# Kernel tuning notes

Hardware: AMD Instinct MI355X
Metric: run time of the kernel (lower is better)

## Reference

```python
import math
import jax, jax.numpy as jnp
import numpy as np

H, W = 24, 24
N = H * W
D = 1024
B = 32
MAX_ITERS = 6

# 9 relative neighbor offsets (3x3 window, row-major)
_REL = np.array([[-1, -1], [-1, 0], [-1, 1], [0, -1], [0, 0], [0, 1], [1, -1], [1, 0], [1, 1]])


def _neighbor_cols():
    y, x = np.meshgrid(np.arange(H), np.arange(W), indexing='ij')
    ny = np.clip(y[None] + _REL[:, 0, None, None], 0, H - 1)  # [9,H,W]
    nx = np.clip(x[None] + _REL[:, 1, None, None], 0, W - 1)
    return jnp.asarray((ny * W + nx).reshape(9, N))  # [9,N]


def setup_inputs() -> dict:
    key = jax.random.key(0)
    ks = jax.random.split(key, 8)
    return {
        'tok2d': jax.random.normal(ks[0], (B, N + 1, D), dtype=jnp.float32),
        'dw_w': jax.random.normal(ks[1], (D, 1, 3, 3), dtype=jnp.float32) * 0.02,
        'pw_w': jax.random.normal(ks[2], (9, D, 1, 1), dtype=jnp.float32) * 0.02,
        'pw_b': jnp.zeros((9,), dtype=jnp.float32),
        'q_w': jax.random.normal(ks[3], (D, D), dtype=jnp.float32) * 0.02,
        'q_b': jax.random.normal(ks[4], (D,), dtype=jnp.float32) * 0.02,
        'v_w': jax.random.normal(ks[5], (D, D), dtype=jnp.float32) * 0.02,
        'v_b': jax.random.normal(ks[6], (D,), dtype=jnp.float32) * 0.02,
        'K': 256,
        'MAX_TOKENS': 128,
    }


def _affinity_head(patch2d, dw_w, pw_w, pw_b):
    # patch2d: [B,H,W,D] -> Q: [B,H,W,9]
    x = jnp.transpose(patch2d, (0, 3, 1, 2))  # NCHW
    x = jax.lax.conv_general_dilated(
        x, dw_w, window_strides=(1, 1), padding='SAME',
        feature_group_count=D,
        dimension_numbers=('NCHW', 'OIHW', 'NCHW'))
    x = jnp.einsum('bdhw,od->bohw', x, pw_w[:, :, 0, 0]) + pw_b[None, :, None, None]
    return jax.nn.softmax(jnp.transpose(x, (0, 2, 3, 1)), axis=-1)


def _build_token_affinity(Q):
    # Q: [B,H,W,9] -> A: [B,N,N] via 9 shifted-neighbor scatters
    cols = _neighbor_cols()                                   # [9,N]
    rows = jnp.broadcast_to(jnp.arange(N)[None, :], (9, N))   # [9,N]
    vals = jnp.moveaxis(Q.reshape(-1, N, 9), -1, 1).reshape(-1, 9 * N)  # [B,9*N]
    A = jnp.zeros((Q.shape[0], N, N), dtype=Q.dtype)
    return A.at[:, rows.reshape(-1), cols.reshape(-1)].add(vals)


def _cluster_roots(A):
    roots = jnp.argmax(A, axis=-1)  # [B,N]
    for _ in range(MAX_ITERS):      # pointer jumping (idempotent once converged)
        roots = jnp.take_along_axis(roots, roots, axis=1)
    return roots


def _cluster_centers(E, roots, K):
    b = E.shape[0]
    bidx = jnp.arange(b)[:, None]
    centers_sum = jnp.zeros_like(E).at[bidx, roots].add(E)          # [B,N,D]
    counts = jnp.zeros(E.shape[:2], E.dtype).at[bidx, roots].add(1.0)  # [B,N]
    _, topk_idx = jax.lax.top_k(counts, K)
    ord_idx = jnp.sort(topk_idx, axis=1)
    cs = jnp.take_along_axis(centers_sum, ord_idx[:, :, None], axis=1)
    cnt = jnp.take_along_axis(counts, ord_idx, axis=1)
    C = cs / jnp.clip(cnt, 1.0, None)[:, :, None]
    return C, cnt


def reference(tok2d, dw_w, pw_w, pw_b, q_w, q_b, v_w, v_b, K, MAX_TOKENS):
    cls_tok = tok2d[:, :1, :]                 # [B,1,D]
    patch = tok2d[:, 1:, :]                   # [B,N,D]
    Q = _affinity_head(patch.reshape(-1, H, W, D), dw_w, pw_w, pw_b)
    A = _build_token_affinity(Q)
    roots = _cluster_roots(A)
    C, cnt = _cluster_centers(patch, roots, K)
    Q_cls = cls_tok @ q_w.T + q_b             # [B,1,D]
    K_v = C @ v_w.T + v_b                     # [B,K,D]
    scores = jnp.einsum('bod,bkd->bk', Q_cls, K_v) / math.sqrt(D)
    valid = jnp.where(cnt > 0, scores, -jnp.inf)
    m = min(MAX_TOKENS, C.shape[1])
    _, idx = jax.lax.top_k(valid, m)
    idx_sorted = jnp.sort(idx, axis=-1)
    return jnp.take_along_axis(C, idx_sorted[:, :, None], axis=1)  # [B,m,D]
```

## Files before the change

kernel.cpp:

```cpp
#include <hip/hip_runtime.h>
#include <math.h>

#define Hh 24
#define Ww 24
#define Nn 576
#define Dd 1024
#define Bb 32
#define Kk 256
#define Mm 128
#define TOKSTRIDE (577 * 1024)

#define R0_OFF 0
#define P_OFF 2944
#define QC_OFF 3776
#define U_OFF 4800
#define T_OFF 5824
#define UP_OFF 6144

__device__ __forceinline__ float* batch_base(float* out, int b) {
  return out + (size_t)b * Mm * Dd;
}

__device__ __forceinline__ float wave_sum_dpp(float x) {
  int y;
  y = __builtin_amdgcn_update_dpp(0, __float_as_int(x), 0x111, 0xf, 0xf, true);
  x += __int_as_float(y);
  y = __builtin_amdgcn_update_dpp(0, __float_as_int(x), 0x112, 0xf, 0xf, true);
  x += __int_as_float(y);
  y = __builtin_amdgcn_update_dpp(0, __float_as_int(x), 0x114, 0xf, 0xf, true);
  x += __int_as_float(y);
  y = __builtin_amdgcn_update_dpp(0, __float_as_int(x), 0x118, 0xf, 0xf, true);
  x += __int_as_float(y);
  y = __builtin_amdgcn_update_dpp(0, __float_as_int(x), 0x142, 0xa, 0xf, true);
  x += __int_as_float(y);
  y = __builtin_amdgcn_update_dpp(0, __float_as_int(x), 0x143, 0xc, 0xf, true);
  x += __int_as_float(y);
  return x;
}

__device__ __forceinline__ float row_sum_dpp(float x) {
  int y;
  y = __builtin_amdgcn_update_dpp(0, __float_as_int(x), 0x111, 0xf, 0xf, true);
  x += __int_as_float(y);
  y = __builtin_amdgcn_update_dpp(0, __float_as_int(x), 0x112, 0xf, 0xf, true);
  x += __int_as_float(y);
  y = __builtin_amdgcn_update_dpp(0, __float_as_int(x), 0x114, 0xf, 0xf, true);
  x += __int_as_float(y);
  y = __builtin_amdgcn_update_dpp(0, __float_as_int(x), 0x118, 0xf, 0xf, true);
  x += __int_as_float(y);
  return x;
}

__global__ __launch_bounds__(256) void qcls_kernel(
    const float* __restrict__ tok2d, const float* __restrict__ q_w,
    const float* __restrict__ q_b, float* __restrict__ outb) {
  int dp = blockIdx.x;
  int wave = threadIdx.x >> 6;
  int lane = threadIdx.x & 63;
  float4 qv[4];
#pragma unroll
  for (int i = 0; i < 4; i++)
    qv[i] = *(const float4*)(q_w + (size_t)dp * Dd + lane * 4 + 256 * i);
  float qb = q_b[dp];
  for (int bb = 0; bb < 8; bb++) {
    int b = wave * 8 + bb;
    const float* cls = tok2d + (size_t)b * TOKSTRIDE;
    float a = 0.f;
#pragma unroll
    for (int i = 0; i < 4; i++) {
      float4 cv = *(const float4*)(cls + lane * 4 + 256 * i);
      a += qv[i].x * cv.x + qv[i].y * cv.y + qv[i].z * cv.z + qv[i].w * cv.w;
    }
    a = wave_sum_dpp(a);
    if (lane == 63) batch_base(outb, b)[QC_OFF + dp] = a + qb;
  }
}

__global__ __launch_bounds__(256) void u_part_kernel(const float* __restrict__ v_w,
                                                     float* __restrict__ outb) {
  int b = blockIdx.x >> 3;
  int chunk = blockIdx.x & 7;
  int tid = threadIdx.x;
  int d0 = tid * 4;
  float* basef = batch_base(outb, b);
  __shared__ float qs[128];
  if (tid < 128) qs[tid] = basef[QC_OFF + chunk * 128 + tid];
  __syncthreads();
  float4 a = make_float4(0.f, 0.f, 0.f, 0.f);
#pragma unroll 4
  for (int dpl = 0; dpl < 128; dpl++) {
    int dp = chunk * 128 + dpl;
    float4 vv = *(const float4*)(v_w + (size_t)dp * Dd + d0);
    float qq = qs[dpl];
    a.x += qq * vv.x; a.y += qq * vv.y; a.z += qq * vv.z; a.w += qq * vv.w;
  }
  *(float4*)(basef + UP_OFF + chunk * Dd + d0) = a;
}

__global__ __launch_bounds__(256) void combine_ut_kernel(
    const float* __restrict__ v_b, float* __restrict__ outb) {
  int b = blockIdx.x;
  int tid = threadIdx.x;
  float* basef = batch_base(outb, b);
  int d0 = tid * 4;
  float4 s = make_float4(0.f, 0.f, 0.f, 0.f);
#pragma unroll
  for (int c = 0; c < 8; c++) {
    float4 v = *(const float4*)(basef + UP_OFF + c * Dd + d0);
    s.x += v.x; s.y += v.y; s.z += v.z; s.w += v.w;
  }
  *(float4*)(basef + U_OFF + d0) = s;

  float a = 0.f;
  for (int i = tid; i < Dd; i += 256) a += basef[QC_OFF + i] * v_b[i];
  __shared__ float sh[256];
  sh[tid] = a;
  __syncthreads();
  for (int st = 128; st > 0; st >>= 1) {
    if (tid < st) sh[tid] += sh[tid + st];
    __syncthreads();
  }
  if (tid == 0) basef[T_OFF] = sh[0];
}

__global__ __launch_bounds__(256, 4) void affinity_p_root_kernel(
    const float* __restrict__ tok2d, const float* __restrict__ dw_w,
    const float* __restrict__ pw_w, const float* __restrict__ pw_b,
    float* __restrict__ outb) {
  int wave = threadIdx.x >> 6;
  int lane = threadIdx.x & 63;
  int blk = (blockIdx.x & 7) * (Bb * Hh * 3 / 8) + (blockIdx.x >> 3);
  int b = blk / (Hh * 3);
  int rem = blk % (Hh * 3);
  int y = rem / 3;
  int x0 = (rem % 3) * 8;
  int d0 = wave * 256 + lane * 4;
  const float* patch = tok2d + (size_t)b * TOKSTRIDE + Dd;
  float* basef = batch_base(outb, b);

  __shared__ float red[8 * 167 + 8];

  union { float4 v[9]; float f[36]; } w;
  const float4* dwp = (const float4*)(dw_w + (size_t)d0 * 9);
#pragma unroll
  for (int j = 0; j < 9; j++) w.v[j] = dwp[j];
  float4 u4 = *(const float4*)(basef + U_OFF + d0);

  float4 cc[8];
  float pacc[8];
#pragma unroll
  for (int t = 0; t < 8; t++) {
    cc[t] = make_float4(0.f, 0.f, 0.f, 0.f);
    pacc[t] = 0.f;
  }
#pragma unroll
  for (int ky = 0; ky < 3; ky++) {
    int yy = y + ky - 1;
    if (yy < 0 || yy >= Hh) continue;
    const float* prow = patch + (size_t)(yy * Ww) * Dd + d0;
    float4 wA = make_float4(0.f, 0.f, 0.f, 0.f);
    if (x0 > 0) wA = *(const float4*)(prow + (size_t)(x0 - 1) * Dd);
    float4 wB = *(const float4*)(prow + (size_t)x0 * Dd);
    int kA = ky * 3, kB = ky * 3 + 1, kC = ky * 3 + 2;
#pragma unroll
    for (int t = 0; t < 8; t++) {
      float4 wC = make_float4(0.f, 0.f, 0.f, 0.f);
      int xx = x0 + t + 1;
      if (xx < Ww) wC = *(const float4*)(prow + (size_t)xx * Dd);
      cc[t].x += wA.x * w.f[kA] + wB.x * w.f[kB] + wC.x * w.f[kC];
      cc[t].y += wA.y * w.f[9 + kA] + wB.y * w.f[9 + kB] + wC.y * w.f[9 + kC];
      cc[t].z += wA.z * w.f[18 + kA] + wB.z * w.f[18 + kB] + wC.z * w.f[18 + kC];
      cc[t].w += wA.w * w.f[27 + kA] + wB.w * w.f[27 + kB] + wC.w * w.f[27 + kC];
      if (ky == 1)
        pacc[t] = wB.x * u4.x + wB.y * u4.y + wB.z * u4.z + wB.w * u4.w;
      wA = wB;
      wB = wC;
    }
  }

  __builtin_amdgcn_sched_barrier(0);

  float4 pw[9];
#pragma unroll
  for (int o = 0; o < 9; o++)
    pw[o] = *(const float4*)(pw_w + (size_t)o * Dd + d0);

#pragma unroll
  for (int t = 0; t < 8; t++) {
    float acc[10];
#pragma unroll
    for (int o = 0; o < 9; o++) {
      acc[o] = cc[t].x * pw[o].x + cc[t].y * pw[o].y + cc[t].z * pw[o].z +
               cc[t].w * pw[o].w;
    }
    acc[9] = pacc[t];
#pragma unroll
    for (int o = 0; o < 10; o++) acc[o] = row_sum_dpp(acc[o]);
    if ((lane & 15) == 15) {
      int r = wave * 4 + (lane >> 4);
#pragma unroll
      for (int o = 0; o < 10; o++) red[t * 167 + r * 10 + o] = acc[o];
    }
  }
  __syncthreads();

  if (lane < 2) {
    int t = wave * 2 + lane;
    int x = x0 + t;
    int n = y * Ww + x;
    float l[10];
#pragma unroll
    for (int o = 0; o < 10; o++) l[o] = 0.f;
    for (int r = 0; r < 16; r++) {
#pragma unroll
      for (int o = 0; o < 10; o++) l[o] += red[t * 167 + r * 10 + o];
    }
    float q[9];
    float mx = -INFINITY;
#pragma unroll
    for (int o = 0; o < 9; o++) {
      l[o] += pw_b[o];
      mx = fmaxf(mx, l[o]);
    }
    float ssum = 0.f;
#pragma unroll
    for (int o = 0; o < 9; o++) {
      q[o] = expf(l[o] - mx);
      ssum += q[o];
    }
#pragma unroll
    for (int o = 0; o < 9; o++) q[o] = q[o] / ssum;

    int colv[9];
#pragma unroll
    for (int o = 0; o < 9; o++) {
      int dy = o / 3 - 1, dx = o % 3 - 1;
      int ny = min(max(y + dy, 0), Hh - 1);
      int nx = min(max(x + dx, 0), Ww - 1);
      colv[o] = ny * Ww + nx;
    }
    float best = -1.f;
    int bcol = 1 << 30;
#pragma unroll
    for (int o = 0; o < 9; o++) {
      float v = 0.f;
#pragma unroll
      for (int oo = 0; oo < 9; oo++)
        v = (colv[oo] == colv[o]) ? v + q[oo] : v;
      if (v > best || (v == best && colv[o] < bcol)) {
        best = v;
        bcol = colv[o];
      }
    }
    ((int*)basef)[R0_OFF + n] = bcol;
    basef[P_OFF + n] = l[9];
  }
}

__global__ __launch_bounds__(576) void cluster_scores_plan_kernel(
    float* __restrict__ outb) {
  int b = blockIdx.x;
  int n = threadIdx.x;
  float* basef = batch_base(outb, b);
  int* base = (int*)basef;
  __shared__ int ra[Nn], rb[Nn], scnt[Nn], soff[Nn], smem[Nn];
  __shared__ float sp[Nn];
  __shared__ int s_ord[Kk], s_cnt[Kk], sel[Kk], s_out[Mm];
  __shared__ float ss[Kk];
  ra[n] = base[R0_OFF + n];
  sp[n] = basef[P_OFF + n];
  scnt[n] = 0;
  __syncthreads();
  for (int it = 0; it < 6; it++) {
    rb[n] = ra[ra[n]];
    __syncthreads();
    ra[n] = rb[n];
    __syncthreads();
  }
  int r = ra[n];
  atomicAdd(&scnt[r], 1);
  __syncthreads();

  soff[n] = scnt[n];
  __syncthreads();
  for (int s = 1; s < Nn; s <<= 1) {
    int v = (n >= s) ? soff[n - s] : 0;
    __syncthreads();
    soff[n] += v;
    __syncthreads();
  }
  int offr = soff[r] - scnt[r];
  int rk = 0;
  for (int m = 0; m < n; m++) rk += (ra[m] == r);
  smem[offr + rk] = n;

  int cn = scnt[n];
  int rank = 0;
  for (int m = 0; m < Nn; m++) {
    int cm = scnt[m];
    rank += (cm > cn) || (cm == cn && m < n);
  }
  int sl = (rank < Kk) ? 1 : 0;
  rb[n] = sl;
  __syncthreads();
  for (int s = 1; s < Nn; s <<= 1) {
    int v = (n >= s) ? rb[n - s] : 0;
    __syncthreads();
    rb[n] += v;
    __syncthreads();
  }
  if (sl) {
    int pos = rb[n] - 1;
    s_ord[pos] = n;
    s_cnt[pos] = cn;
  }
  __syncthreads();

  if (n < Kk) {
    int idx = s_ord[n];
    int c = s_cnt[n];
    float s;
    if (c > 0) {
      int off = soff[idx] - scnt[idx];
      float sum = 0.f;
      for (int j = 0; j < c; j++) sum += sp[smem[off + j]];
      s = (sum / (float)c + basef[T_OFF]) * (1.0f / 32.0f);
    } else {
      s = -INFINITY;
    }
    ss[n] = s;
  }
  __syncthreads();

  if (n < Kk) {
    float vk = ss[n];
    int rank2 = 0;
    for (int m = 0; m < Kk; m++) {
      float vm = ss[m];
      rank2 += (vm > vk) || (vm == vk && m < n);
    }
    sel[n] = (rank2 < Mm) ? 1 : 0;
  }
  __syncthreads();
  if (n < Kk && sel[n]) {
    int pos = 0;
    for (int m = 0; m < n; m++) pos += sel[m];
    s_out[pos] = n;
  }
  __syncthreads();

  int w9 = n >> 6, lane = n & 63;
  for (int kp = w9; kp < Mm; kp += 9) {
    int k = s_out[kp];
    int kidx = s_ord[k];
    int kc = s_cnt[k];
    int koff = soff[kidx] - scnt[kidx];
    int* row = base + kp * Dd;
    if (lane == 0) row[0] = kc;
    for (int j = lane; j < kc; j += 64) row[1 + j] = smem[koff + j];
  }
}

__global__ __launch_bounds__(256) void output_kernel(
    const float* __restrict__ tok2d, float* __restrict__ outb) {
  int blk = blockIdx.x;
  int b = blk / Mm;
  int tid = threadIdx.x;
  float* rowf = outb + (size_t)blk * Dd;
  int* rowi = (int*)rowf;
  __shared__ int s_c;
  __shared__ int s_m[Nn];
  if (tid == 0) s_c = rowi[0];
  __syncthreads();
  int c = s_c;
  for (int j = tid; j < c; j += 256) s_m[j] = rowi[1 + j];
  __syncthreads();
  const float* patch = tok2d + (size_t)b * TOKSTRIDE + Dd;
  int d0 = tid * 4;
  float4 acc = make_float4(0.f, 0.f, 0.f, 0.f);
  for (int j = 0; j < c; j++) {
    float4 rv = *(const float4*)(patch + (size_t)s_m[j] * Dd + d0);
    acc.x += rv.x; acc.y += rv.y; acc.z += rv.z; acc.w += rv.w;
  }
  float inv = 1.0f / (float)max(c, 1);
  *(float4*)(rowf + d0) =
      make_float4(acc.x * inv, acc.y * inv, acc.z * inv, acc.w * inv);
}

extern "C" void kernel_launch(void* const* d_in, const int* in_sizes, int n_in,
                              void* d_out, int out_size, void* d_ws,
                              size_t ws_size, hipStream_t stream) {
  const float* tok2d = (const float*)d_in[0];
  const float* dw_w = (const float*)d_in[1];
  const float* pw_w = (const float*)d_in[2];
  const float* pw_b = (const float*)d_in[3];
  const float* q_w = (const float*)d_in[4];
  const float* q_b = (const float*)d_in[5];
  const float* v_w = (const float*)d_in[6];
  const float* v_b = (const float*)d_in[7];
  float* out = (float*)d_out;
  (void)d_ws; (void)ws_size;

  qcls_kernel<<<dim3(Dd), dim3(256), 0, stream>>>(tok2d, q_w, q_b, out);
  u_part_kernel<<<dim3(Bb * 8), dim3(256), 0, stream>>>(v_w, out);
  combine_ut_kernel<<<dim3(Bb), dim3(256), 0, stream>>>(v_b, out);
  affinity_p_root_kernel<<<dim3(Bb * Hh * 3), dim3(256), 0, stream>>>(
      tok2d, dw_w, pw_w, pw_b, out);
  cluster_scores_plan_kernel<<<dim3(Bb), dim3(Nn), 0, stream>>>(out);
  output_kernel<<<dim3(Bb * Mm), dim3(256), 0, stream>>>(tok2d, out);
}
```

Baseline: 239.1 us.

## Fuse U partial/combine kernels and batch row loads in depthwise conv

Merges u_part and combine_ut into one kernel. Each block now covers a 128-wide output slice and reduces across the input dimension in shared memory, which removes one launch and the global partial-sum buffer. The depthwise conv loop now loads all 10 row vectors up front instead of streaming them one by one, to expose more memory-level parallelism. Occupancy in launch_bounds drops from 4 to 3 to make room for the extra registers.

```diff
diff --git a/kernel.cpp b/kernel.cpp
--- a/kernel.cpp
+++ b/kernel.cpp
@@ -15,7 +15,6 @@
 #define QC_OFF 3776
 #define U_OFF 4800
 #define T_OFF 5824
-#define UP_OFF 6144
 
 __device__ __forceinline__ float* batch_base(float* out, int b) {
   return out + (size_t)b * Mm * Dd;
@@ -76,54 +75,55 @@
   }
 }
 
-__global__ __launch_bounds__(256) void u_part_kernel(const float* __restrict__ v_w,
-                                                     float* __restrict__ outb) {
+__global__ __launch_bounds__(256) void u_t_kernel(const float* __restrict__ v_w,
+                                                  const float* __restrict__ v_b,
+                                                  float* __restrict__ outb) {
   int b = blockIdx.x >> 3;
-  int chunk = blockIdx.x & 7;
+  int s = blockIdx.x & 7;
   int tid = threadIdx.x;
-  int d0 = tid * 4;
+  int dl = tid & 31;
+  int g = tid >> 5;
   float* basef = batch_base(outb, b);
-  __shared__ float qs[128];
-  if (tid < 128) qs[tid] = basef[QC_OFF + chunk * 128 + tid];
-  __syncthreads();
+  __shared__ float qs[Dd];
+  __shared__ float4 part[8][32];
+  __shared__ float sh[256];
+  for (int i = tid; i < Dd; i += 256) qs[i] = basef[QC_OFF + i];
+  __syncthreads();
+  int d0 = s * 128 + dl * 4;
   float4 a = make_float4(0.f, 0.f, 0.f, 0.f);
 #pragma unroll 4
   for (int dpl = 0; dpl < 128; dpl++) {
-    int dp = chunk * 128 + dpl;
+    int dp = g * 128 + dpl;
     float4 vv = *(const float4*)(v_w + (size_t)dp * Dd + d0);
-    float qq = qs[dpl];
+    float qq = qs[dp];
     a.x += qq * vv.x; a.y += qq * vv.y; a.z += qq * vv.z; a.w += qq * vv.w;
   }
-  *(float4*)(basef + UP_OFF + chunk * Dd + d0) = a;
-}
-
-__global__ __launch_bounds__(256) void combine_ut_kernel(
-    const float* __restrict__ v_b, float* __restrict__ outb) {
-  int b = blockIdx.x;
-  int tid = threadIdx.x;
-  float* basef = batch_base(outb, b);
-  int d0 = tid * 4;
-  float4 s = make_float4(0.f, 0.f, 0.f, 0.f);
-#pragma unroll
-  for (int c = 0; c < 8; c++) {
-    float4 v = *(const float4*)(basef + UP_OFF + c * Dd + d0);
-    s.x += v.x; s.y += v.y; s.z += v.z; s.w += v.w;
-  }
-  *(float4*)(basef + U_OFF + d0) = s;
-
-  float a = 0.f;
-  for (int i = tid; i < Dd; i += 256) a += basef[QC_OFF + i] * v_b[i];
-  __shared__ float sh[256];
-  sh[tid] = a;
-  __syncthreads();
-  for (int st = 128; st > 0; st >>= 1) {
-    if (tid < st) sh[tid] += sh[tid + st];
-    __syncthreads();
-  }
-  if (tid == 0) basef[T_OFF] = sh[0];
-}
-
-__global__ __launch_bounds__(256, 4) void affinity_p_root_kernel(
+  part[g][dl] = a;
+  __syncthreads();
+  if (tid < 32) {
+    float4 u = make_float4(0.f, 0.f, 0.f, 0.f);
+#pragma unroll
+    for (int c = 0; c < 8; c++) {
+      float4 v = part[c][tid];
+      u.x += v.x; u.y += v.y; u.z += v.z; u.w += v.w;
+    }
+    *(float4*)(basef + U_OFF + s * 128 + tid * 4) = u;
+  }
+
+  if (s == 0) {
+    float aa = 0.f;
+    for (int i = tid; i < Dd; i += 256) aa += qs[i] * v_b[i];
+    sh[tid] = aa;
+    __syncthreads();
+    for (int st = 128; st > 0; st >>= 1) {
+      if (tid < st) sh[tid] += sh[tid + st];
+      __syncthreads();
+    }
+    if (tid == 0) basef[T_OFF] = sh[0];
+  }
+}
+
+__global__ __launch_bounds__(256, 3) void affinity_p_root_kernel(
     const float* __restrict__ tok2d, const float* __restrict__ dw_w,
     const float* __restrict__ pw_w, const float* __restrict__ pw_b,
     float* __restrict__ outb) {
@@ -158,23 +158,28 @@
     int yy = y + ky - 1;
     if (yy < 0 || yy >= Hh) continue;
     const float* prow = patch + (size_t)(yy * Ww) * Dd + d0;
-    float4 wA = make_float4(0.f, 0.f, 0.f, 0.f);
-    if (x0 > 0) wA = *(const float4*)(prow + (size_t)(x0 - 1) * Dd);
-    float4 wB = *(const float4*)(prow + (size_t)x0 * Dd);
+    float4 wrow[10];
+    wrow[0] = make_float4(0.f, 0.f, 0.f, 0.f);
+    if (x0 > 0) wrow[0] = *(const float4*)(prow + (size_t)(x0 - 1) * Dd);
+#pragma unroll
+    for (int j = 1; j < 9; j++)
+      wrow[j] = *(const float4*)(prow + (size_t)(x0 - 1 + j) * Dd);
+    wrow[9] = make_float4(0.f, 0.f, 0.f, 0.f);
+    if (x0 + 8 < Ww) wrow[9] = *(const float4*)(prow + (size_t)(x0 + 8) * Dd);
     int kA = ky * 3, kB = ky * 3 + 1, kC = ky * 3 + 2;
 #pragma unroll
     for (int t = 0; t < 8; t++) {
-      float4 wC = make_float4(0.f, 0.f, 0.f, 0.f);
-      int xx = x0 + t + 1;
-      if (xx < Ww) wC = *(const float4*)(prow + (size_t)xx * Dd);
-      cc[t].x += wA.x * w.f[kA] + wB.x * w.f[kB] + wC.x * w.f[kC];
-      cc[t].y += wA.y * w.f[9 + kA] + wB.y * w.f[9 + kB] + wC.y * w.f[9 + kC];
-      cc[t].z += wA.z * w.f[18 + kA] + wB.z * w.f[18 + kB] + wC.z * w.f[18 + kC];
-      cc[t].w += wA.w * w.f[27 + kA] + wB.w * w.f[27 + kB] + wC.w * w.f[27 + kC];
+      cc[t].x += wrow[t].x * w.f[kA] + wrow[t + 1].x * w.f[kB] +
+                 wrow[t + 2].x * w.f[kC];
+      cc[t].y += wrow[t].y * w.f[9 + kA] + wrow[t + 1].y * w.f[9 + kB] +
+                 wrow[t + 2].y * w.f[9 + kC];
+      cc[t].z += wrow[t].z * w.f[18 + kA] + wrow[t + 1].z * w.f[18 + kB] +
+                 wrow[t + 2].z * w.f[18 + kC];
+      cc[t].w += wrow[t].w * w.f[27 + kA] + wrow[t + 1].w * w.f[27 + kB] +
+                 wrow[t + 2].w * w.f[27 + kC];
       if (ky == 1)
-        pacc[t] = wB.x * u4.x + wB.y * u4.y + wB.z * u4.z + wB.w * u4.w;
-      wA = wB;
-      wB = wC;
+        pacc[t] = wrow[t + 1].x * u4.x + wrow[t + 1].y * u4.y +
+                  wrow[t + 1].z * u4.z + wrow[t + 1].w * u4.w;
     }
   }
 
@@ -402,8 +407,7 @@
   (void)d_ws; (void)ws_size;
 
   qcls_kernel<<<dim3(Dd), dim3(256), 0, stream>>>(tok2d, q_w, q_b, out);
-  u_part_kernel<<<dim3(Bb * 8), dim3(256), 0, stream>>>(v_w, out);
-  combine_ut_kernel<<<dim3(Bb), dim3(256), 0, stream>>>(v_b, out);
+  u_t_kernel<<<dim3(Bb * 8), dim3(256), 0, stream>>>(v_w, v_b, out);
   affinity_p_root_kernel<<<dim3(Bb * Hh * 3), dim3(256), 0, stream>>>(
       tok2d, dw_w, pw_w, pw_b, out);
   cluster_scores_plan_kernel<<<dim3(Bb), dim3(Nn), 0, stream>>>(out);
```

New measurement: 232.8 us. 2.7% less time.
